# Optimization experiments

Measured on AMD Instinct MI355X. Metric: run time of the kernel, lower is better.

The kernel has to match this reference:

```python
import jax, jax.numpy as jnp
import numpy as np

T, B, IN, H = 256, 128, 512, 1024


def setup_inputs() -> dict:
    key = jax.random.key(0)
    ks = jax.random.split(key, 13)
    s = 1.0 / float(np.sqrt(H))  # torch LSTMCell init: U(-1/sqrt(H), 1/sqrt(H))
    u = lambda k, shp: jax.random.uniform(k, shp, jnp.float32, -s, s)
    return {
        "x": jax.random.normal(ks[0], (T, B, IN), jnp.float32),
        "h0_fwd": jax.random.normal(ks[1], (B, H), jnp.float32),
        "c0_fwd": jax.random.normal(ks[2], (B, H), jnp.float32),
        "h0_rev": jax.random.normal(ks[3], (B, H), jnp.float32),
        "c0_rev": jax.random.normal(ks[4], (B, H), jnp.float32),
        "W_ih_f": u(ks[5], (4 * H, IN)),
        "W_hh_f": u(ks[6], (4 * H, H)),
        "b_ih_f": u(ks[7], (4 * H,)),
        "b_hh_f": u(ks[8], (4 * H,)),
        "W_ih_r": u(ks[9], (4 * H, IN)),
        "W_hh_r": u(ks[10], (4 * H, H)),
        "b_ih_r": u(ks[11], (4 * H,)),
        "b_hh_r": u(ks[12], (4 * H,)),
    }


def _lstm(x, h0, c0, Wih, Whh, bih, bhh, reverse):
    # Precompute the input projection for all timesteps in one big GEMM.
    xp = jnp.einsum('tbi,gi->tbg', x, Wih) + bih + bhh  # [T, B, 4H]

    def step(carry, xg):
        h, c = carry
        gates = xg + h @ Whh.T  # [B, 4H]
        i, f, g, o = jnp.split(gates, 4, axis=-1)  # torch gate order: i, f, g, o
        c = jax.nn.sigmoid(f) * c + jax.nn.sigmoid(i) * jnp.tanh(g)
        h = jax.nn.sigmoid(o) * jnp.tanh(c)
        return (h, c), h

    # reverse=True scans backward in time but emits outputs in original order,
    # exactly matching ReverseLSTMLayer's reverse-process-then-reverse-outputs.
    (h, c), ys = jax.lax.scan(step, (h0, c0), xp, reverse=reverse)
    return ys, h, c


def reference(x, h0_fwd, c0_fwd, h0_rev, c0_rev,
              W_ih_f, W_hh_f, b_ih_f, b_hh_f,
              W_ih_r, W_hh_r, b_ih_r, b_hh_r):
    yf, hf, cf = _lstm(x, h0_fwd, c0_fwd, W_ih_f, W_hh_f, b_ih_f, b_hh_f, False)
    yr, hr, cr = _lstm(x, h0_rev, c0_rev, W_ih_r, W_hh_r, b_ih_r, b_hh_r, True)
    out = jnp.concatenate([yf, yr], axis=-1)  # [T, B, 2H]
    # Faithful to the original's `hidden, cell = output_states` quirk:
    # `hidden` is the forward direction's (h, c) pair stacked,
    # `cell` is the reverse direction's (h, c) pair stacked.
    hidden = jnp.stack([hf, cf])  # [2, B, H]
    cell = jnp.stack([hr, cr])    # [2, B, H]
    return out, (hidden, cell)
```

## Files before the change

kernel.cpp:

```cpp
#include <hip/hip_runtime.h>
#include <hip/hip_bf16.h>

typedef unsigned short u16;
typedef __attribute__((ext_vector_type(8))) short bf16x8;
typedef __attribute__((ext_vector_type(8))) u16   u16x8;
typedef __attribute__((ext_vector_type(4))) float f32x4;

#define T_STEPS 256
#define BATCH   128
#define INDIM   512
#define HDIM    1024
#define GDIM    4096
#define KTOT    1536

#define OFF_XBF   ((size_t)0)
#define XBF_BYTES ((size_t)T_STEPS * BATCH * INDIM * 2)
#define OFF_BM    (OFF_XBF + XBF_BYTES)
#define BM_BYTES  ((size_t)2 * GDIM * KTOT * 2)
#define OFF_BIAS  (OFF_BM + BM_BYTES)
#define BIAS_BYTES ((size_t)2 * GDIM * 4)
#define OFF_CNT   (OFF_BIAS + BIAS_BYTES)
#define OFF_ROLL  (OFF_CNT + 8192)
#define ROLL_BYTES ((size_t)(T_STEPS + 1) * 2 * BATCH * HDIM * 2)
#define WS_NEED   (OFF_ROLL + ROLL_BYTES)

__device__ __forceinline__ u16 f2b(float f) {
  __hip_bfloat16 h = __float2bfloat16(f);
  return *reinterpret_cast<u16*>(&h);
}

__device__ __forceinline__ void glds16(const void* g, void* l) {
  __builtin_amdgcn_global_load_lds(
      (const __attribute__((address_space(1))) unsigned int*)g,
      (__attribute__((address_space(3))) unsigned int*)l, 16, 0, 0);
}

__global__ void k_cast_x(const float* __restrict__ x, u16* __restrict__ xs) {
  int i = blockIdx.x * 256 + threadIdx.x;
  int t   = i >> 13;
  int r13 = i & 8191;
  int row = r13 >> 6;
  int c0  = (r13 & 63) * 8;
  int q = row >> 5, rloc = row & 31;
  int mi = rloc >> 4, ar = rloc & 15;
  int kq = c0 >> 7, kr = c0 & 127;
  int ks = kr >> 5, h4 = (kr & 31) >> 3;
  int lane = h4 * 16 + ar;
  const float* src = x + ((size_t)t * BATCH + row) * INDIM + c0;
  f32x4 a = *reinterpret_cast<const f32x4*>(src);
  f32x4 b = *reinterpret_cast<const f32x4*>(src + 4);
  u16x8 u;
  u[0] = f2b(a[0]); u[1] = f2b(a[1]); u[2] = f2b(a[2]); u[3] = f2b(a[3]);
  u[4] = f2b(b[0]); u[5] = f2b(b[1]); u[6] = f2b(b[2]); u[7] = f2b(b[3]);
  size_t dst = ((((((size_t)t * 4 + q) * 4 + kq) * 4 + ks) * 2 + mi) * 64 + lane) * 8;
  *reinterpret_cast<u16x8*>(xs + dst) = u;
}

__global__ void k_build_b(const float* __restrict__ Whh_f, const float* __restrict__ Wih_f,
                          const float* __restrict__ Whh_r, const float* __restrict__ Wih_r,
                          u16* __restrict__ Bm) {
  int blk = blockIdx.x;
  int dir = blk >> 5, jt = blk & 31;
  const float* Whh = dir ? Whh_r : Whh_f;
  const float* Wih = dir ? Wih_r : Wih_f;
  u16* dst = Bm + (size_t)blk * 128 * KTOT;
  for (int c = 0; c < 128; c++) {
    int G = (c >> 5) * HDIM + jt * 32 + (c & 31);
    for (int k = threadIdx.x; k < KTOT; k += 256) {
      float v = (k < HDIM) ? Whh[(size_t)G * HDIM + k] : Wih[(size_t)G * INDIM + (k - HDIM)];
      dst[c * KTOT + k] = f2b(v);
    }
  }
}

__global__ void k_init(const float* __restrict__ h0f, const float* __restrict__ h0r,
                       const float* __restrict__ bihf, const float* __restrict__ bhhf,
                       const float* __restrict__ bihr, const float* __restrict__ bhhr,
                       u16* __restrict__ hroll, float* __restrict__ bias,
                       unsigned* __restrict__ flags) {
  int i = blockIdx.x * 256 + threadIdx.x;
  if (i < 2 * BATCH * HDIM) {
    int dir = i / (BATCH * HDIM);
    int rem = i - dir * BATCH * HDIM;
    int r = rem / HDIM, c = rem - r * HDIM;
    const float* h0 = dir ? h0r : h0f;
    char* hb = (char*)hroll;
    *(u16*)(hb + ((size_t)dir * BATCH + r) * 2048 + ((2 * c) ^ ((r & 7) << 4))) =
        f2b(h0[rem]);
  }
  if (i < 2 * GDIM) {
    int dir = i / GDIM, g = i - dir * GDIM;
    bias[i] = dir ? (bihr[g] + bhhr[g]) : (bihf[g] + bhhf[g]);
  }
  if (i < 512) flags[i] = 0;
}

__global__ __launch_bounds__(512, 2) void k_lstm(
    const u16* __restrict__ xs, const u16* __restrict__ Bm,
    u16* __restrict__ hroll,
    const float* __restrict__ bias, unsigned* __restrict__ flags,
    const float* __restrict__ c0f, const float* __restrict__ c0r,
    float* __restrict__ out) {
  __shared__ float ldsf[34816];
  char* ldsc = reinterpret_cast<char*>(ldsf);
  float* ldsP = ldsf + 16384;

  __builtin_amdgcn_fence(__ATOMIC_ACQUIRE, "agent");

  const int wg   = blockIdx.x;
  const int grp  = wg & 7;
  const int dir  = grp >> 2, q = grp & 3;
  const int jt32 = wg >> 3;
  const int tid  = threadIdx.x;
  const int w = tid >> 6, lane = tid & 63;
  const int kq = w >> 1, nh = w & 1;
  const int h4 = lane >> 4, kk = h4 * 8;
  const int ar = lane & 15;

  const u16* bsrc = Bm + (size_t)(dir * 32 + jt32) * 128 * KTOT;
  bf16x8 bh[8][4], bx[4][4];
#pragma unroll
  for (int ks = 0; ks < 8; ks++)
#pragma unroll
    for (int ni = 0; ni < 4; ni++)
      bh[ks][ni] = *reinterpret_cast<const bf16x8*>(
          bsrc + (size_t)(nh * 64 + ni * 16 + ar) * KTOT + 256 * kq + 32 * ks + kk);
#pragma unroll
  for (int ks = 0; ks < 4; ks++)
#pragma unroll
    for (int ni = 0; ni < 4; ni++)
      bx[ks][ni] = *reinterpret_cast<const bf16x8*>(
          bsrc + (size_t)(nh * 64 + ni * 16 + ar) * KTOT + HDIM + 128 * kq + 32 * ks + kk);

  const int rrow = tid & 31;
  const int jl0  = 2 * (tid >> 5);
  const int row0 = q * 32 + rrow;
  const int jg0  = jt32 * 32 + jl0;
  const float* c0 = dir ? c0r : c0f;
  float2 cc = *reinterpret_cast<const float2*>(c0 + (size_t)row0 * HDIM + jg0);
  float cst0 = cc.x, cst1 = cc.y;
  const float2 b_i = *reinterpret_cast<const float2*>(bias + dir * GDIM + 0 * HDIM + jg0);
  const float2 b_f = *reinterpret_cast<const float2*>(bias + dir * GDIM + 1 * HDIM + jg0);
  const float2 b_g = *reinterpret_cast<const float2*>(bias + dir * GDIM + 2 * HDIM + jg0);
  const float2 b_o = *reinterpret_cast<const float2*>(bias + dir * GDIM + 3 * HDIM + jg0);

  const unsigned* fpA = flags + grp * 32 + (lane & 31);

#pragma unroll 1
  for (int s = 0; s < T_STEPS; s++) {
    const int t = dir ? (T_STEPS - 1 - s) : s;

    bf16x8 ax[4][2];
    {
      const u16* xb = xs + ((((size_t)t * 4 + q) * 4 + kq) * 4) * 2 * 512;
#pragma unroll
      for (int ks = 0; ks < 4; ks++)
#pragma unroll
        for (int mi = 0; mi < 2; mi++)
          ax[ks][mi] = *reinterpret_cast<const bf16x8*>(
              xb + ((size_t)(ks * 2 + mi) * 64 + lane) * 8);
    }

    if (s > 0) {
      while (true) {
        unsigned f = __hip_atomic_load(fpA, __ATOMIC_RELAXED, __HIP_MEMORY_SCOPE_AGENT);
        if (__all((int)(f >= (unsigned)s))) break;
        __builtin_amdgcn_s_sleep(1);
      }
      __builtin_amdgcn_sched_barrier(0);
    }

    {
      const char* hRd = (const char*)hroll + ((size_t)s * 2 + dir) * (BATCH * 2048)
                        + (size_t)q * 32 * 2048;
      unsigned off = (unsigned)tid * 16;
#pragma unroll
      for (int i = 0; i < 8; i++)
        glds16(hRd + off + i * 8192, ldsc + off + i * 8192);
    }
    __builtin_amdgcn_sched_barrier(0);

    f32x4 acc[2][4];
#pragma unroll
    for (int mi = 0; mi < 2; mi++)
#pragma unroll
      for (int ni = 0; ni < 4; ni++) acc[mi][ni] = f32x4{0.f, 0.f, 0.f, 0.f};
#pragma unroll
    for (int ks = 0; ks < 4; ks++)
#pragma unroll
      for (int mi = 0; mi < 2; mi++)
#pragma unroll
        for (int ni = 0; ni < 4; ni++)
          acc[mi][ni] = __builtin_amdgcn_mfma_f32_16x16x32_bf16(ax[ks][mi], bx[ks][ni], acc[mi][ni], 0, 0, 0);

    __syncthreads();

#pragma unroll
    for (int ks = 0; ks < 8; ks++) {
      bf16x8 af[2];
#pragma unroll
      for (int mi = 0; mi < 2; mi++) {
        unsigned row = 16 * mi + ar;
        unsigned cb = (256 * kq + 32 * ks + kk) * 2;
        af[mi] = *reinterpret_cast<const bf16x8*>(
            ldsc + row * 2048 + (cb ^ ((row & 7) << 4)));
      }
#pragma unroll
      for (int mi = 0; mi < 2; mi++)
#pragma unroll
        for (int ni = 0; ni < 4; ni++)
          acc[mi][ni] = __builtin_amdgcn_mfma_f32_16x16x32_bf16(af[mi], bh[ks][ni], acc[mi][ni], 0, 0, 0);
    }

    {
      float* pw = ldsP + kq * (128 * 36);
#pragma unroll
      for (int mi = 0; mi < 2; mi++)
#pragma unroll
        for (int ni = 0; ni < 4; ni++) {
          int col = nh * 64 + ni * 16 + ar;
          *reinterpret_cast<f32x4*>(pw + col * 36 + mi * 16 + h4 * 4) = acc[mi][ni];
        }
    }
    __syncthreads();

    float h0v, h1v;
    {
      float gi0 = b_i.x, gi1 = b_i.y, gf0 = b_f.x, gf1 = b_f.y;
      float gg0 = b_g.x, gg1 = b_g.y, go0 = b_o.x, go1 = b_o.y;
#pragma unroll
      for (int k4 = 0; k4 < 4; k4++) {
        const float* p = ldsP + k4 * (128 * 36);
        gi0 += p[(0 * 32 + jl0) * 36 + rrow]; gi1 += p[(0 * 32 + jl0 + 1) * 36 + rrow];
        gf0 += p[(1 * 32 + jl0) * 36 + rrow]; gf1 += p[(1 * 32 + jl0 + 1) * 36 + rrow];
        gg0 += p[(2 * 32 + jl0) * 36 + rrow]; gg1 += p[(2 * 32 + jl0 + 1) * 36 + rrow];
        go0 += p[(3 * 32 + jl0) * 36 + rrow]; go1 += p[(3 * 32 + jl0 + 1) * 36 + rrow];
      }
      float i0 = 1.f / (1.f + __expf(-gi0)), i1 = 1.f / (1.f + __expf(-gi1));
      float f0 = 1.f / (1.f + __expf(-gf0)), f1 = 1.f / (1.f + __expf(-gf1));
      float g0 = tanhf(gg0), g1 = tanhf(gg1);
      float o0 = 1.f / (1.f + __expf(-go0)), o1 = 1.f / (1.f + __expf(-go1));
      cst0 = f0 * cst0 + i0 * g0;
      cst1 = f1 * cst1 + i1 * g1;
      h0v = o0 * tanhf(cst0);
      h1v = o1 * tanhf(cst1);

      unsigned hp = (unsigned)f2b(h0v) | ((unsigned)f2b(h1v) << 16);
      char* hb = (char*)hroll + ((size_t)(s + 1) * 2 + dir) * (BATCH * 2048);
      __hip_atomic_store(
          (unsigned*)(hb + (size_t)row0 * 2048 + ((2 * jg0) ^ ((row0 & 7) << 4))),
          hp, __ATOMIC_RELAXED, __HIP_MEMORY_SCOPE_AGENT);
    }

    asm volatile("s_waitcnt vmcnt(0)" ::: "memory");
    __syncthreads();
    if (tid == 0)
      __hip_atomic_store(flags + grp * 32 + jt32, (unsigned)(s + 1),
                         __ATOMIC_RELAXED, __HIP_MEMORY_SCOPE_AGENT);

    {
      float2 yv; yv.x = h0v; yv.y = h1v;
      *reinterpret_cast<float2*>(out + ((size_t)t * BATCH + row0) * (2 * HDIM)
                                     + (size_t)dir * HDIM + jg0) = yv;
      if (s == T_STEPS - 1) {
        size_t hid = (size_t)T_STEPS * BATCH * 2 * HDIM;
        size_t base2 = hid + (size_t)dir * 2 * BATCH * HDIM;
        *reinterpret_cast<float2*>(out + base2 + (size_t)row0 * HDIM + jg0) = yv;
        float2 cv; cv.x = cst0; cv.y = cst1;
        *reinterpret_cast<float2*>(out + base2 + (size_t)BATCH * HDIM
                                       + (size_t)row0 * HDIM + jg0) = cv;
      }
    }
  }
}

extern "C" void kernel_launch(void* const* d_in, const int* in_sizes, int n_in,
                              void* d_out, int out_size, void* d_ws, size_t ws_size,
                              hipStream_t stream) {
  const float* x     = (const float*)d_in[0];
  const float* h0f   = (const float*)d_in[1];
  const float* c0f   = (const float*)d_in[2];
  const float* h0r   = (const float*)d_in[3];
  const float* c0r   = (const float*)d_in[4];
  const float* Wih_f = (const float*)d_in[5];
  const float* Whh_f = (const float*)d_in[6];
  const float* bih_f = (const float*)d_in[7];
  const float* bhh_f = (const float*)d_in[8];
  const float* Wih_r = (const float*)d_in[9];
  const float* Whh_r = (const float*)d_in[10];
  const float* bih_r = (const float*)d_in[11];
  const float* bhh_r = (const float*)d_in[12];
  float* out = (float*)d_out;
  char* ws = (char*)d_ws;

  if (ws_size < WS_NEED) return;

  u16* xsf        = (u16*)(ws + OFF_XBF);
  u16* Bm         = (u16*)(ws + OFF_BM);
  float* bias     = (float*)(ws + OFF_BIAS);
  unsigned* flags = (unsigned*)(ws + OFF_CNT);
  u16* hroll      = (u16*)(ws + OFF_ROLL);

  k_cast_x<<<8192, 256, 0, stream>>>(x, xsf);
  k_build_b<<<64, 256, 0, stream>>>(Whh_f, Wih_f, Whh_r, Wih_r, Bm);
  k_init<<<1024, 256, 0, stream>>>(h0f, h0r, bih_f, bhh_f, bih_r, bhh_r,
                                   hroll, bias, flags);
  k_lstm<<<256, 512, 0, stream>>>(xsf, Bm, hroll, bias, flags, c0f, c0r, out);
}
```

Measured before the change: 2.292 ms.

## Store hidden state in MFMA fragment layout and load directly to registers

The hidden state is now written to global memory in the exact MFMA A-fragment order, so each wave loads its h operands straight into registers. This removes the global-to-LDS copy and one block-wide barrier per timestep. Each wave now waits only on the 8 producer flags covering its K-quarter instead of all 32. The gate-reduction thread mapping and LDS pad (36 to 37) also change. In exchange, direct global loads may expose more latency per step than the LDS path did.

```diff
diff --git a/kernel.cpp b/kernel.cpp
--- a/kernel.cpp
+++ b/kernel.cpp
@@ -24,15 +24,10 @@
 #define ROLL_BYTES ((size_t)(T_STEPS + 1) * 2 * BATCH * HDIM * 2)
 #define WS_NEED   (OFF_ROLL + ROLL_BYTES)
 
+
 __device__ __forceinline__ u16 f2b(float f) {
   __hip_bfloat16 h = __float2bfloat16(f);
   return *reinterpret_cast<u16*>(&h);
-}
-
-__device__ __forceinline__ void glds16(const void* g, void* l) {
-  __builtin_amdgcn_global_load_lds(
-      (const __attribute__((address_space(1))) unsigned int*)g,
-      (__attribute__((address_space(3))) unsigned int*)l, 16, 0, 0);
 }
 
 __global__ void k_cast_x(const float* __restrict__ x, u16* __restrict__ xs) {
@@ -76,17 +71,20 @@
 __global__ void k_init(const float* __restrict__ h0f, const float* __restrict__ h0r,
                        const float* __restrict__ bihf, const float* __restrict__ bhhf,
                        const float* __restrict__ bihr, const float* __restrict__ bhhr,
-                       u16* __restrict__ hroll, float* __restrict__ bias,
+                       u16* __restrict__ hfrag, float* __restrict__ bias,
                        unsigned* __restrict__ flags) {
   int i = blockIdx.x * 256 + threadIdx.x;
   if (i < 2 * BATCH * HDIM) {
     int dir = i / (BATCH * HDIM);
     int rem = i - dir * BATCH * HDIM;
     int r = rem / HDIM, c = rem - r * HDIM;
+    int q = r >> 5, rloc = r & 31;
+    int mi = rloc >> 4, ar = rloc & 15;
+    int kq = c >> 8, ks = (c >> 5) & 7, h4 = (c & 31) >> 3, e = c & 7;
     const float* h0 = dir ? h0r : h0f;
-    char* hb = (char*)hroll;
-    *(u16*)(hb + ((size_t)dir * BATCH + r) * 2048 + ((2 * c) ^ ((r & 7) << 4))) =
-        f2b(h0[rem]);
+    size_t off = ((size_t)(dir * 4 + q)) * 32768
+               + (((size_t)(kq * 8 + ks) * 2 + mi) * 64 + h4 * 16 + ar) * 8 + e;
+    hfrag[off] = f2b(h0[rem]);
   }
   if (i < 2 * GDIM) {
     int dir = i / GDIM, g = i - dir * GDIM;
@@ -97,13 +95,11 @@
 
 __global__ __launch_bounds__(512, 2) void k_lstm(
     const u16* __restrict__ xs, const u16* __restrict__ Bm,
-    u16* __restrict__ hroll,
+    u16* __restrict__ hfrag,
     const float* __restrict__ bias, unsigned* __restrict__ flags,
     const float* __restrict__ c0f, const float* __restrict__ c0r,
     float* __restrict__ out) {
-  __shared__ float ldsf[34816];
-  char* ldsc = reinterpret_cast<char*>(ldsf);
-  float* ldsP = ldsf + 16384;
+  __shared__ float ldsP[4 * 128 * 37];
 
   __builtin_amdgcn_fence(__ATOMIC_ACQUIRE, "agent");
 
@@ -132,8 +128,8 @@
       bx[ks][ni] = *reinterpret_cast<const bf16x8*>(
           bsrc + (size_t)(nh * 64 + ni * 16 + ar) * KTOT + HDIM + 128 * kq + 32 * ks + kk);
 
-  const int rrow = tid & 31;
-  const int jl0  = 2 * (tid >> 5);
+  const int rrow = tid >> 4;
+  const int jl0  = 2 * (tid & 15);
   const int row0 = q * 32 + rrow;
   const int jg0  = jt32 * 32 + jl0;
   const float* c0 = dir ? c0r : c0f;
@@ -144,7 +140,11 @@
   const float2 b_g = *reinterpret_cast<const float2*>(bias + dir * GDIM + 2 * HDIM + jg0);
   const float2 b_o = *reinterpret_cast<const float2*>(bias + dir * GDIM + 3 * HDIM + jg0);
 
-  const unsigned* fpA = flags + grp * 32 + (lane & 31);
+  const int pmi = rrow >> 4, par = rrow & 15;
+  const int ph4 = jl0 >> 3, pe = jl0 & 7;
+  const size_t poff = (((size_t)(jt32 * 2 + pmi) * 64 + ph4 * 16 + par) * 8 + pe);
+
+  const unsigned* fpw = flags + grp * 32 + 8 * kq + (lane & 7);
 
 #pragma unroll 1
   for (int s = 0; s < T_STEPS; s++) {
@@ -163,63 +163,58 @@
 
     if (s > 0) {
       while (true) {
-        unsigned f = __hip_atomic_load(fpA, __ATOMIC_RELAXED, __HIP_MEMORY_SCOPE_AGENT);
+        unsigned f = __hip_atomic_load(fpw, __ATOMIC_RELAXED, __HIP_MEMORY_SCOPE_AGENT);
         if (__all((int)(f >= (unsigned)s))) break;
         __builtin_amdgcn_s_sleep(1);
       }
       __builtin_amdgcn_sched_barrier(0);
     }
 
+    f32x4 acc[2][4];
+#pragma unroll
+    for (int mi = 0; mi < 2; mi++)
+#pragma unroll
+      for (int ni = 0; ni < 4; ni++) acc[mi][ni] = f32x4{0.f, 0.f, 0.f, 0.f};
+
+    const u16* hB = hfrag + ((size_t)s * 8 + dir * 4 + q) * 32768;
+#pragma unroll
+    for (int half = 0; half < 2; half++) {
+      bf16x8 ah[4][2];
+#pragma unroll
+      for (int k2 = 0; k2 < 4; k2++)
+#pragma unroll
+        for (int mi = 0; mi < 2; mi++) {
+          int ks = half * 4 + k2;
+          ah[k2][mi] = *reinterpret_cast<const bf16x8*>(
+              hB + (((size_t)(kq * 8 + ks) * 2 + mi) * 64 + lane) * 8);
+        }
+      if (half == 0) {
+#pragma unroll
+        for (int ks = 0; ks < 4; ks++)
+#pragma unroll
+          for (int mi = 0; mi < 2; mi++)
+#pragma unroll
+            for (int ni = 0; ni < 4; ni++)
+              acc[mi][ni] = __builtin_amdgcn_mfma_f32_16x16x32_bf16(ax[ks][mi], bx[ks][ni], acc[mi][ni], 0, 0, 0);
+      }
+#pragma unroll
+      for (int k2 = 0; k2 < 4; k2++)
+#pragma unroll
+        for (int mi = 0; mi < 2; mi++)
+#pragma unroll
+          for (int ni = 0; ni < 4; ni++)
+            acc[mi][ni] = __builtin_amdgcn_mfma_f32_16x16x32_bf16(
+                ah[k2][mi], bh[half * 4 + k2][ni], acc[mi][ni], 0, 0, 0);
+    }
+
     {
-      const char* hRd = (const char*)hroll + ((size_t)s * 2 + dir) * (BATCH * 2048)
-                        + (size_t)q * 32 * 2048;
-      unsigned off = (unsigned)tid * 16;
-#pragma unroll
-      for (int i = 0; i < 8; i++)
-        glds16(hRd + off + i * 8192, ldsc + off + i * 8192);
-    }
-    __builtin_amdgcn_sched_barrier(0);
-
-    f32x4 acc[2][4];
-#pragma unroll
-    for (int mi = 0; mi < 2; mi++)
-#pragma unroll
-      for (int ni = 0; ni < 4; ni++) acc[mi][ni] = f32x4{0.f, 0.f, 0.f, 0.f};
-#pragma unroll
-    for (int ks = 0; ks < 4; ks++)
-#pragma unroll
-      for (int mi = 0; mi < 2; mi++)
-#pragma unroll
-        for (int ni = 0; ni < 4; ni++)
-          acc[mi][ni] = __builtin_amdgcn_mfma_f32_16x16x32_bf16(ax[ks][mi], bx[ks][ni], acc[mi][ni], 0, 0, 0);
-
-    __syncthreads();
-
-#pragma unroll
-    for (int ks = 0; ks < 8; ks++) {
-      bf16x8 af[2];
-#pragma unroll
-      for (int mi = 0; mi < 2; mi++) {
-        unsigned row = 16 * mi + ar;
-        unsigned cb = (256 * kq + 32 * ks + kk) * 2;
-        af[mi] = *reinterpret_cast<const bf16x8*>(
-            ldsc + row * 2048 + (cb ^ ((row & 7) << 4)));
-      }
-#pragma unroll
-      for (int mi = 0; mi < 2; mi++)
-#pragma unroll
-        for (int ni = 0; ni < 4; ni++)
-          acc[mi][ni] = __builtin_amdgcn_mfma_f32_16x16x32_bf16(af[mi], bh[ks][ni], acc[mi][ni], 0, 0, 0);
-    }
-
-    {
-      float* pw = ldsP + kq * (128 * 36);
+      float* pw = ldsP + kq * (128 * 37);
 #pragma unroll
       for (int mi = 0; mi < 2; mi++)
 #pragma unroll
         for (int ni = 0; ni < 4; ni++) {
           int col = nh * 64 + ni * 16 + ar;
-          *reinterpret_cast<f32x4*>(pw + col * 36 + mi * 16 + h4 * 4) = acc[mi][ni];
+          *reinterpret_cast<f32x4*>(pw + col * 37 + mi * 16 + h4 * 4) = acc[mi][ni];
         }
     }
     __syncthreads();
@@ -230,11 +225,11 @@
       float gg0 = b_g.x, gg1 = b_g.y, go0 = b_o.x, go1 = b_o.y;
 #pragma unroll
       for (int k4 = 0; k4 < 4; k4++) {
-        const float* p = ldsP + k4 * (128 * 36);
-        gi0 += p[(0 * 32 + jl0) * 36 + rrow]; gi1 += p[(0 * 32 + jl0 + 1) * 36 + rrow];
-        gf0 += p[(1 * 32 + jl0) * 36 + rrow]; gf1 += p[(1 * 32 + jl0 + 1) * 36 + rrow];
-        gg0 += p[(2 * 32 + jl0) * 36 + rrow]; gg1 += p[(2 * 32 + jl0 + 1) * 36 + rrow];
-        go0 += p[(3 * 32 + jl0) * 36 + rrow]; go1 += p[(3 * 32 + jl0 + 1) * 36 + rrow];
+        const float* p = ldsP + k4 * (128 * 37);
+        gi0 += p[(0 * 32 + jl0) * 37 + rrow]; gi1 += p[(0 * 32 + jl0 + 1) * 37 + rrow];
+        gf0 += p[(1 * 32 + jl0) * 37 + rrow]; gf1 += p[(1 * 32 + jl0 + 1) * 37 + rrow];
+        gg0 += p[(2 * 32 + jl0) * 37 + rrow]; gg1 += p[(2 * 32 + jl0 + 1) * 37 + rrow];
+        go0 += p[(3 * 32 + jl0) * 37 + rrow]; go1 += p[(3 * 32 + jl0 + 1) * 37 + rrow];
       }
       float i0 = 1.f / (1.f + __expf(-gi0)), i1 = 1.f / (1.f + __expf(-gi1));
       float f0 = 1.f / (1.f + __expf(-gf0)), f1 = 1.f / (1.f + __expf(-gf1));
@@ -246,10 +241,9 @@
       h1v = o1 * tanhf(cst1);
 
       unsigned hp = (unsigned)f2b(h0v) | ((unsigned)f2b(h1v) << 16);
-      char* hb = (char*)hroll + ((size_t)(s + 1) * 2 + dir) * (BATCH * 2048);
-      __hip_atomic_store(
-          (unsigned*)(hb + (size_t)row0 * 2048 + ((2 * jg0) ^ ((row0 & 7) << 4))),
-          hp, __ATOMIC_RELAXED, __HIP_MEMORY_SCOPE_AGENT);
+      u16* hD = hfrag + ((size_t)(s + 1) * 8 + dir * 4 + q) * 32768;
+      __hip_atomic_store(reinterpret_cast<unsigned*>(hD + poff),
+                         hp, __ATOMIC_RELAXED, __HIP_MEMORY_SCOPE_AGENT);
     }
 
     asm volatile("s_waitcnt vmcnt(0)" ::: "memory");
@@ -299,11 +293,11 @@
   u16* Bm         = (u16*)(ws + OFF_BM);
   float* bias     = (float*)(ws + OFF_BIAS);
   unsigned* flags = (unsigned*)(ws + OFF_CNT);
-  u16* hroll      = (u16*)(ws + OFF_ROLL);
+  u16* hfrag      = (u16*)(ws + OFF_ROLL);
 
   k_cast_x<<<8192, 256, 0, stream>>>(x, xsf);
   k_build_b<<<64, 256, 0, stream>>>(Whh_f, Wih_f, Whh_r, Wih_r, Bm);
   k_init<<<1024, 256, 0, stream>>>(h0f, h0r, bih_f, bhh_f, bih_r, bhh_r,
-                                   hroll, bias, flags);
-  k_lstm<<<256, 512, 0, stream>>>(xsf, Bm, hroll, bias, flags, c0f, c0r, out);
-}
+                                   hfrag, bias, flags);
+  k_lstm<<<256, 512, 0, stream>>>(xsf, Bm, hfrag, bias, flags, c0f, c0r, out);
+}
```

Result: no change. 2.323 ms (+1.4%).
